# Performance work log

Hardware: AMD Instinct MI355X
Metric: run time of the kernel (lower is better)

Reference implementation:

```python
import jax, jax.numpy as jnp
import numpy as np

NUM_HEADS = 4
NUM_EXPERTS = 8
TOP_K = 2
AUX_W = 0.1


def setup_inputs() -> dict:
    key = jax.random.key(0)
    ks = jax.random.split(key, 16)
    B, W, C, T = 32, 64, 27, 2000
    E_EEG, H, S = 200, 256, 768
    D2 = 2 * H  # MoE input/hidden dim = 512
    s = 0.02

    def p(k, shape):
        return (jax.random.normal(k, shape, jnp.float32) * s)

    z = lambda *shape: jnp.zeros(shape, jnp.float32)
    return {
        "eeg_windows": jax.random.normal(ks[0], (B, W, C, T), jnp.float32),
        "padding_mask": jnp.zeros((B, W), bool),
        "smiles_emb": jax.random.normal(ks[1], (B, S), jnp.float32),
        # window encoder (linear stand-in): flatten (C*T) -> E_EEG
        "enc_W": p(ks[2], (C * T, E_EEG)), "enc_b": z(E_EEG),
        # aggregator (masked-mean + linear stand-in): E_EEG -> H
        "agg_W": p(ks[3], (E_EEG, H)), "agg_b": z(H),
        # smiles projection
        "smiles_W": p(ks[4], (S, H)), "smiles_b": z(H),
        # cross attention
        "Wq": p(ks[5], (H, H)), "bq": z(H),
        "Wk": p(ks[6], (H, H)), "bk": z(H),
        "Wv": p(ks[7], (H, H)), "bv": z(H),
        "Wo": p(ks[8], (H, H)), "bo": z(H),
        # MoE gate + experts
        "gate_W": p(ks[9], (D2, NUM_EXPERTS)), "gate_b": z(NUM_EXPERTS),
        "exp_W1": p(ks[10], (NUM_EXPERTS, D2, D2)), "exp_b1": z(NUM_EXPERTS, D2),
        "exp_W2": p(ks[11], (NUM_EXPERTS, D2, H)), "exp_b2": z(NUM_EXPERTS, H),
        # classifier
        "ln_g": jnp.ones((H,), jnp.float32), "ln_b": z(H),
        "cls_W": p(ks[12], (H, 2)), "cls_b": z(2),
    }


def reference(eeg_windows, padding_mask, smiles_emb, enc_W, enc_b, agg_W, agg_b,
              smiles_W, smiles_b, Wq, bq, Wk, bk, Wv, bv, Wo, bo,
              gate_W, gate_b, exp_W1, exp_b1, exp_W2, exp_b2,
              ln_g, ln_b, cls_W, cls_b):
    B, W, C, T = eeg_windows.shape
    H = agg_W.shape[1]
    dh = H // NUM_HEADS

    # --- window encoding (stand-in linear encoder) ---
    wemb = eeg_windows.reshape(B, W, C * T) @ enc_W + enc_b  # (B, W, E_EEG)

    # --- aggregator: masked mean pool over windows, then project ---
    valid = (~padding_mask).astype(wemb.dtype)[..., None]      # (B, W, 1)
    pooled = (wemb * valid).sum(1) / jnp.maximum(valid.sum(1), 1.0)
    eeg_emb = pooled @ agg_W + agg_b                           # (B, H)

    smiles_proj = smiles_emb @ smiles_W + smiles_b             # (B, H)

    # --- cross attention (single query token over single kv token) ---
    q = (eeg_emb @ Wq + bq).reshape(B, NUM_HEADS, dh)
    k = (smiles_proj @ Wk + bk).reshape(B, NUM_HEADS, dh)
    v = (smiles_proj @ Wv + bv).reshape(B, NUM_HEADS, dh)
    scores = (q * k).sum(-1, keepdims=True) / jnp.sqrt(jnp.float32(dh))
    attn = jnp.exp(scores - scores)  # softmax over a single key == 1
    attended = (attn * v).reshape(B, H) @ Wo + bo              # (B, H)

    fused = jnp.concatenate([attended, smiles_proj], axis=-1)  # (B, 2H)

    # --- sparse MoE: dense experts, top-k gate, gather, combine ---
    gate_probs = jax.nn.softmax(fused @ gate_W + gate_b, axis=-1)  # (B, E)
    topk_p, topk_i = jax.lax.top_k(gate_probs, TOP_K)
    topk_p = topk_p / topk_p.sum(-1, keepdims=True)
    h1 = jax.nn.gelu(jnp.einsum('bd,edh->beh', fused, exp_W1) + exp_b1,
                     approximate=False)
    expert_out = jnp.einsum('beh,eho->beo', h1, exp_W2) + exp_b2   # (B, E, H)
    sel = jnp.take_along_axis(expert_out, topk_i[:, :, None], axis=1)
    moe_out = (sel * topk_p[..., None]).sum(1)                     # (B, H)

    usage = gate_probs.mean(0)
    uniform = jnp.ones_like(usage) / usage.shape[-1]
    aux = (usage * jnp.log(uniform) - jnp.log(usage) * uniform).sum()

    # --- classifier: LayerNorm + Linear ---
    mu = moe_out.mean(-1, keepdims=True)
    var = moe_out.var(-1, keepdims=True)
    xn = (moe_out - mu) / jnp.sqrt(var + 1e-5)
    logits = (xn * ln_g + ln_b) @ cls_W + cls_b                    # (B, 2)
    return logits, aux * AUX_W
```

## Files before the change

### kernel.cpp

```cpp
#include <hip/hip_runtime.h>
#include <math.h>

#define HD 256
#define SD 768
#define D2 512
#define NE 8
#define NB 32
#define NBLK 256
#define NTHR 256
#define SFP 516

typedef float f32x4 __attribute__((ext_vector_type(4)));
typedef unsigned u32x4 __attribute__((ext_vector_type(4)));

__device__ __forceinline__ float gelu_exact(float x) {
    return 0.5f * x * (1.0f + erff(x * 0.70710678118654752f));
}

__device__ __forceinline__ void cstf(float* p, float v) {
    __hip_atomic_store(p, v, __ATOMIC_RELAXED, __HIP_MEMORY_SCOPE_AGENT);
}
__device__ __forceinline__ float cldf(const float* p) {
    return __hip_atomic_load(p, __ATOMIC_RELAXED, __HIP_MEMORY_SCOPE_AGENT);
}
__device__ __forceinline__ void csti(int* p, int v) {
    __hip_atomic_store(p, v, __ATOMIC_RELAXED, __HIP_MEMORY_SCOPE_AGENT);
}
__device__ __forceinline__ int cldi(const int* p) {
    return __hip_atomic_load(p, __ATOMIC_RELAXED, __HIP_MEMORY_SCOPE_AGENT);
}

__device__ __forceinline__ void stage16k(const float* __restrict__ gsrc,
                                         float* __restrict__ lds, int t)
{
    const f32x4* src = (const f32x4*)gsrc;
    f32x4 r[16];
    #pragma unroll
    for (int j = 0; j < 16; ++j) {
        const f32x4* p = src + (t + j * 256);
        asm volatile("global_load_dwordx4 %0, %1, off sc0 sc1"
                     : "=v"(r[j]) : "v"(p));
    }
    asm volatile("s_waitcnt vmcnt(0)" ::: "memory");
    __builtin_amdgcn_sched_barrier(0);
    #pragma unroll
    for (int j = 0; j < 16; ++j) {
        int q = t + j * 256;
        *(f32x4*)&lds[(q >> 7) * SFP + (q & 127) * 4] = r[j];
    }
}

__device__ __forceinline__ void gsync(unsigned* slots, unsigned* gen,
                                      unsigned tok) {
    __syncthreads();
    const int t = threadIdx.x;
    if (t == 0)
        __hip_atomic_store(slots + blockIdx.x, tok, __ATOMIC_RELAXED,
                           __HIP_MEMORY_SCOPE_AGENT);
    if (blockIdx.x == 0) {
        if (t < 64) {
            const u32x4* p = (const u32x4*)slots + t;
            for (;;) {
                u32x4 v;
                asm volatile("global_load_dwordx4 %0, %1, off sc0 sc1\n\t"
                             "s_waitcnt vmcnt(0)"
                             : "=&v"(v) : "v"(p) : "memory");
                bool ok = (v[0] == tok) & (v[1] == tok) &
                          (v[2] == tok) & (v[3] == tok);
                if (__ballot(ok) == ~0ull) break;
                __builtin_amdgcn_s_sleep(1);
            }
            if (t == 0)
                __hip_atomic_store(gen, tok, __ATOMIC_RELAXED,
                                   __HIP_MEMORY_SCOPE_AGENT);
        }
    } else {
        if (t == 0) {
            while (__hip_atomic_load(gen, __ATOMIC_RELAXED,
                                     __HIP_MEMORY_SCOPE_AGENT) != tok)
                __builtin_amdgcn_s_sleep(1);
        }
    }
    __builtin_amdgcn_fence(__ATOMIC_ACQUIRE, "workgroup");
    __syncthreads();
}

#define S_F     0
#define S_W     16512
#define S_R2    (16512 + 8192)
#define S_RED   (16512 + 8192 + 2048)
#define S_SMALL (16512 + 8192 + 2048 + 256)
#define SMEM_F  (16512 + 8192 + 2048 + 256 + 16)

__global__ __launch_bounds__(256) void fused_all(
    const float* __restrict__ smiles,
    const float* __restrict__ sW, const float* __restrict__ sb,
    const float* __restrict__ Wv, const float* __restrict__ bv,
    const float* __restrict__ Wo, const float* __restrict__ bo,
    const float* __restrict__ gW, const float* __restrict__ gb,
    const float* __restrict__ W1, const float* __restrict__ b1,
    const float* __restrict__ W2, const float* __restrict__ b2,
    const float* __restrict__ lng, const float* __restrict__ lnb,
    const float* __restrict__ clsW, const float* __restrict__ clsb,
    float* __restrict__ proj, float* __restrict__ fused,
    float* __restrict__ probs, float* __restrict__ pn,
    int* __restrict__ sel, float* __restrict__ h1,
    float* __restrict__ eo, unsigned* __restrict__ slots,
    unsigned* __restrict__ gen, unsigned* __restrict__ LC,
    float* __restrict__ out)
{
    __shared__ __align__(16) float smem[SMEM_F];
    __shared__ unsigned s_lc;
    const int bid = blockIdx.x, t = threadIdx.x;

    if (t == 0)
        s_lc = __hip_atomic_load(LC, __ATOMIC_RELAXED, __HIP_MEMORY_SCOPE_AGENT);
    __syncthreads();
    const unsigned tb = s_lc * 2654435761u;

    {
        int r = bid >> 3, sl = bid & 7;
        float* s_in = smem + S_F;
        float* s_red = smem + S_RED;
        const float* srow = smiles + (size_t)r * SD;
        for (int i = t; i < SD / 4; i += NTHR)
            ((float4*)s_in)[i] = ((const float4*)srow)[i];
        __syncthreads();
        int c = t & 31, kq = t >> 5;
        float acc = 0.f;
        const float* wp = sW + (size_t)(kq * 96) * HD + sl * 32 + c;
        #pragma unroll 8
        for (int k = 0; k < 96; ++k)
            acc = fmaf(s_in[kq * 96 + k], wp[(size_t)k * HD], acc);
        s_red[t] = acc;
        __syncthreads();
        if (t < 32) {
            float s = 0.f;
            #pragma unroll
            for (int q = 0; q < 8; ++q) s += s_red[q * 32 + t];
            int col = sl * 32 + t;
            s += sb[col];
            cstf(proj + r * HD + col, s);
            cstf(fused + (size_t)r * 2 * HD + HD + col, s);
        }
    }
    gsync(slots + 0 * NBLK, gen + 0, tb + 1u);

    if (bid < NB) {
        int b = bid;
        float* s_p   = smem + S_F;
        float* s_v   = smem + S_F + 256;
        float* s_f2  = smem + S_F + 512;
        float* s_acc = smem + S_R2;
        float* s_red = smem + S_RED;
        float* s_gate = smem + S_SMALL;
        s_p[t] = cldf(proj + b * HD + t);
        __syncthreads();
        int ks = t >> 6, cg = t & 63;

        f32x4 av = {0.f, 0.f, 0.f, 0.f};
        #pragma unroll 16
        for (int kk = 0; kk < 64; ++kk) {
            int k = ks * 64 + kk;
            f32x4 w = *(const f32x4*)(Wv + (size_t)k * HD + cg * 4);
            av += s_p[k] * w;
        }
        *(f32x4*)&s_acc[ks * 256 + cg * 4] = av;
        __syncthreads();
        s_v[t] = s_acc[t] + s_acc[256 + t] + s_acc[512 + t] + s_acc[768 + t]
               + bv[t];
        __syncthreads();

        f32x4 ao = {0.f, 0.f, 0.f, 0.f};
        #pragma unroll 16
        for (int kk = 0; kk < 64; ++kk) {
            int k = ks * 64 + kk;
            f32x4 w = *(const f32x4*)(Wo + (size_t)k * HD + cg * 4);
            ao += s_v[k] * w;
        }
        *(f32x4*)&s_acc[ks * 256 + cg * 4] = ao;
        __syncthreads();
        float att = s_acc[t] + s_acc[256 + t] + s_acc[512 + t] + s_acc[768 + t]
                  + bo[t];
        s_f2[t] = att;
        s_f2[HD + t] = s_p[t];
        cstf(fused + (size_t)b * 2 * HD + t, att);
        __syncthreads();

        int e = t & 7, ch = t >> 3;
        float gp = 0.f;
        #pragma unroll
        for (int j = 0; j < 16; ++j) {
            int d = ch * 16 + j;
            gp = fmaf(s_f2[d], gW[d * NE + e], gp);
        }
        s_red[t] = gp;
        __syncthreads();
        for (int off = 128; off >= 8; off >>= 1) {
            if (t < off) s_red[t] += s_red[t + off];
            __syncthreads();
        }
        if (t < NE) s_gate[t] = s_red[t] + gb[t];
        __syncthreads();
        if (t == 0) {
            float m = s_gate[0];
            for (int i = 1; i < NE; ++i) m = fmaxf(m, s_gate[i]);
            float ex[NE], ssum = 0.f;
            for (int i = 0; i < NE; ++i) { ex[i] = expf(s_gate[i] - m); ssum += ex[i]; }
            float pr[NE];
            for (int i = 0; i < NE; ++i) { pr[i] = ex[i] / ssum; cstf(probs + b * NE + i, pr[i]); }
            int i1 = 0;
            for (int i = 1; i < NE; ++i) if (pr[i] > pr[i1]) i1 = i;
            int i2 = (i1 == 0) ? 1 : 0;
            for (int i = 0; i < NE; ++i) if (i != i1 && pr[i] > pr[i2]) i2 = i;
            float p1 = pr[i1], p2 = pr[i2], s12 = p1 + p2;
            csti(sel + b * 2 + 0, i1);
            csti(sel + b * 2 + 1, i2);
            cstf(pn + b * 2 + 0, p1 / s12);
            cstf(pn + b * 2 + 1, p2 / s12);
        }
    }
    gsync(slots + 1 * NBLK, gen + 1, tb + 2u);

    {
        int e = bid >> 5, ct = bid & 31;
        float* s_f  = smem + S_F;
        float* s_w  = smem + S_W;
        float* s_r2 = smem + S_R2;
        stage16k(fused, s_f, t);
        {
            const float* Wb = W1 + (size_t)e * D2 * D2 + ct * 16;
            #pragma unroll
            for (int j = 0; j < 8; ++j) {
                int q = t + j * 256;
                int k = q >> 2, c4 = (q & 3) * 4;
                *(float4*)&s_w[k * 16 + c4] =
                    *(const float4*)(Wb + (size_t)k * D2 + c4);
            }
        }
        __syncthreads();
        int ks = t >> 6, l = t & 63;
        int rp = l >> 2, c4g = l & 3;
        int r0 = rp * 2, r1 = r0 + 1;
        const float* fr0 = s_f + r0 * SFP;
        const float* fr1 = s_f + r1 * SFP;
        const float* wb = s_w + c4g * 4;
        f32x4 a0 = {0.f, 0.f, 0.f, 0.f}, a1 = {0.f, 0.f, 0.f, 0.f};
        #pragma unroll 4
        for (int kq = 0; kq < 32; ++kq) {
            int k = ks * 128 + kq * 4;
            f32x4 w0 = *(const f32x4*)&wb[(k + 0) * 16];
            f32x4 w1 = *(const f32x4*)&wb[(k + 1) * 16];
            f32x4 w2 = *(const f32x4*)&wb[(k + 2) * 16];
            f32x4 w3 = *(const f32x4*)&wb[(k + 3) * 16];
            f32x4 f0 = *(const f32x4*)&fr0[k];
            f32x4 f1 = *(const f32x4*)&fr1[k];
            a0 += f0[0] * w0 + f0[1] * w1 + f0[2] * w2 + f0[3] * w3;
            a1 += f1[0] * w0 + f1[1] * w1 + f1[2] * w2 + f1[3] * w3;
        }
        int cl = c4g * 4;
        #pragma unroll
        for (int j = 0; j < 4; ++j) {
            s_r2[(r0 * 16 + cl + j) * 4 + ks] = a0[j];
            s_r2[(r1 * 16 + cl + j) * 4 + ks] = a1[j];
        }
        __syncthreads();
        #pragma unroll
        for (int o = 0; o < 2; ++o) {
            int outi = t * 2 + o;
            f32x4 p = *(const f32x4*)&s_r2[outi * 4];
            int r = outi >> 4, cl2 = outi & 15;
            int col = ct * 16 + cl2;
            float v = p[0] + p[1] + p[2] + p[3] + b1[e * D2 + col];
            cstf(h1 + ((size_t)e * NB + r) * D2 + col, gelu_exact(v));
        }
    }
    gsync(slots + 2 * NBLK, gen + 2, tb + 3u);

    if (bid < 128) {
        int e = bid >> 4, ct = bid & 15;
        float* s_h  = smem + S_F;
        float* s_w  = smem + S_W;
        float* s_r2 = smem + S_R2;
        stage16k(h1 + (size_t)e * NB * D2, s_h, t);
        {
            const float* Wb = W2 + (size_t)e * D2 * HD + ct * 16;
            #pragma unroll
            for (int j = 0; j < 8; ++j) {
                int q = t + j * 256;
                int k = q >> 2, c4 = (q & 3) * 4;
                *(float4*)&s_w[k * 16 + c4] =
                    *(const float4*)(Wb + (size_t)k * HD + c4);
            }
        }
        __syncthreads();
        int ks = t >> 6, l = t & 63;
        int rp = l >> 2, c4g = l & 3;
        int r0 = rp * 2, r1 = r0 + 1;
        const float* fr0 = s_h + r0 * SFP;
        const float* fr1 = s_h + r1 * SFP;
        const float* wb = s_w + c4g * 4;
        f32x4 a0 = {0.f, 0.f, 0.f, 0.f}, a1 = {0.f, 0.f, 0.f, 0.f};
        #pragma unroll 4
        for (int kq = 0; kq < 32; ++kq) {
            int k = ks * 128 + kq * 4;
            f32x4 w0 = *(const f32x4*)&wb[(k + 0) * 16];
            f32x4 w1 = *(const f32x4*)&wb[(k + 1) * 16];
            f32x4 w2 = *(const f32x4*)&wb[(k + 2) * 16];
            f32x4 w3 = *(const f32x4*)&wb[(k + 3) * 16];
            f32x4 f0 = *(const f32x4*)&fr0[k];
            f32x4 f1 = *(const f32x4*)&fr1[k];
            a0 += f0[0] * w0 + f0[1] * w1 + f0[2] * w2 + f0[3] * w3;
            a1 += f1[0] * w0 + f1[1] * w1 + f1[2] * w2 + f1[3] * w3;
        }
        int cl = c4g * 4;
        #pragma unroll
        for (int j = 0; j < 4; ++j) {
            s_r2[(r0 * 16 + cl + j) * 4 + ks] = a0[j];
            s_r2[(r1 * 16 + cl + j) * 4 + ks] = a1[j];
        }
        __syncthreads();
        #pragma unroll
        for (int o = 0; o < 2; ++o) {
            int outi = t * 2 + o;
            f32x4 p = *(const f32x4*)&s_r2[outi * 4];
            int r = outi >> 4, cl2 = outi & 15;
            int col = ct * 16 + cl2;
            float v = p[0] + p[1] + p[2] + p[3] + b2[e * HD + col];
            cstf(eo + ((size_t)e * NB + r) * HD + col, v);
        }
    }
    gsync(slots + 3 * NBLK, gen + 3, tb + 4u);

    if (bid == 0 && t == 0)
        __hip_atomic_store(LC, s_lc + 1u, __ATOMIC_RELAXED, __HIP_MEMORY_SCOPE_AGENT);

    if (bid < NB) {
        int b = bid;
        float* s_red = smem + S_RED;
        float* s_stats = smem + S_SMALL;
        int e0 = cldi(sel + b * 2 + 0), e1 = cldi(sel + b * 2 + 1);
        float p0 = cldf(pn + b * 2 + 0), p1 = cldf(pn + b * 2 + 1);
        float moe = p0 * cldf(eo + ((size_t)e0 * NB + b) * HD + t)
                  + p1 * cldf(eo + ((size_t)e1 * NB + b) * HD + t);

        s_red[t] = moe; __syncthreads();
        for (int off = 128; off > 0; off >>= 1) {
            if (t < off) s_red[t] += s_red[t + off];
            __syncthreads();
        }
        if (t == 0) s_stats[0] = s_red[0] * (1.f / HD);
        __syncthreads();
        float mu = s_stats[0];
        float d = moe - mu;

        s_red[t] = d * d; __syncthreads();
        for (int off = 128; off > 0; off >>= 1) {
            if (t < off) s_red[t] += s_red[t + off];
            __syncthreads();
        }
        if (t == 0) s_stats[1] = s_red[0] * (1.f / HD);
        __syncthreads();

        float xn = d * rsqrtf(s_stats[1] + 1e-5f);
        float y = fmaf(xn, lng[t], lnb[t]);

        s_red[t] = y * clsW[t * 2 + 0]; __syncthreads();
        for (int off = 128; off > 0; off >>= 1) {
            if (t < off) s_red[t] += s_red[t + off];
            __syncthreads();
        }
        if (t == 0) s_stats[2] = s_red[0] + clsb[0];
        __syncthreads();

        s_red[t] = y * clsW[t * 2 + 1]; __syncthreads();
        for (int off = 128; off > 0; off >>= 1) {
            if (t < off) s_red[t] += s_red[t + off];
            __syncthreads();
        }
        if (t == 0) {
            out[b * 2 + 0] = s_stats[2];
            out[b * 2 + 1] = s_red[0] + clsb[1];
        }

        if (bid == 0) {
            __syncthreads();
            s_red[t] = cldf(probs + t);
            __syncthreads();
            for (int off = 128; off >= 8; off >>= 1) {
                if (t < off) s_red[t] += s_red[t + off];
                __syncthreads();
            }
            if (t == 0) {
                float aux = 0.f;
                for (int e = 0; e < NE; ++e) {
                    float u = s_red[e] * (1.f / 32.f);
                    aux += u * logf(0.125f) - logf(u) * 0.125f;
                }
                out[64] = 0.1f * aux;
            }
        }
    }
}

extern "C" void kernel_launch(void* const* d_in, const int* in_sizes, int n_in,
                              void* d_out, int out_size, void* d_ws, size_t ws_size,
                              hipStream_t stream) {
    (void)in_sizes; (void)n_in; (void)out_size; (void)ws_size;
    const float* smiles = (const float*)d_in[2];
    const float* sW  = (const float*)d_in[7];
    const float* sb  = (const float*)d_in[8];
    const float* Wv  = (const float*)d_in[13];
    const float* bv  = (const float*)d_in[14];
    const float* Wo  = (const float*)d_in[15];
    const float* bo  = (const float*)d_in[16];
    const float* gW  = (const float*)d_in[17];
    const float* gb  = (const float*)d_in[18];
    const float* W1  = (const float*)d_in[19];
    const float* b1  = (const float*)d_in[20];
    const float* W2  = (const float*)d_in[21];
    const float* b2  = (const float*)d_in[22];
    const float* lng = (const float*)d_in[23];
    const float* lnb = (const float*)d_in[24];
    const float* cW  = (const float*)d_in[25];
    const float* cb  = (const float*)d_in[26];
    float* out = (float*)d_out;
    float* ws  = (float*)d_ws;

    float*    proj  = ws;
    float*    fused = ws + 8192;
    float*    probs = ws + 24576;
    float*    pn    = ws + 24832;
    int*      sel   = (int*)(ws + 24896);
    float*    h1    = ws + 24960;
    float*    eo    = ws + 156032;
    unsigned* slots = (unsigned*)(ws + 221568);
    unsigned* LC    = (unsigned*)(ws + 222592);
    unsigned* gen   = (unsigned*)(ws + 222593);

    fused_all<<<NBLK, NTHR, 0, stream>>>(
        smiles, sW, sb, Wv, bv, Wo, bo, gW, gb, W1, b1, W2, b2,
        lng, lnb, cW, cb,
        proj, fused, probs, pn, sel, h1, eo, slots, gen, LC, out);
}
```

Baseline: 41.64 us.

## Merge smiles projection into attention phase and compute only top-k expert W2

The smiles projection moves into the per-batch attention blocks, so 32 blocks each compute a full 768x256 projection row and one grid barrier is removed. The dense second expert layer and its barrier are also dropped. Each batch block now loads the h1 rows for its two selected experts, scales them by the gate weights and multiplies by those experts' W2 directly. This cuts the grid-wide syncs from four to two and skips the six unselected experts' W2 work. The cost is more serial per-block work, since 32 blocks stream sW and W2 from global memory instead of spreading that work across 256 blocks.

Result: slower. 48.03 us (+15.3%).

```diff
diff --git a/kernel.cpp b/kernel.cpp
--- a/kernel.cpp
+++ b/kernel.cpp
@@ -28,6 +28,12 @@
 }
 __device__ __forceinline__ int cldi(const int* p) {
     return __hip_atomic_load(p, __ATOMIC_RELAXED, __HIP_MEMORY_SCOPE_AGENT);
+}
+__device__ __forceinline__ f32x4 cld4(const float* p) {
+    f32x4 v;
+    asm volatile("global_load_dwordx4 %0, %1, off sc0 sc1\n\t"
+                 "s_waitcnt vmcnt(0)" : "=&v"(v) : "v"(p) : "memory");
+    return v;
 }
 
 __device__ __forceinline__ void stage16k(const float* __restrict__ gsrc,
@@ -102,10 +108,9 @@
     const float* __restrict__ W2, const float* __restrict__ b2,
     const float* __restrict__ lng, const float* __restrict__ lnb,
     const float* __restrict__ clsW, const float* __restrict__ clsb,
-    float* __restrict__ proj, float* __restrict__ fused,
-    float* __restrict__ probs, float* __restrict__ pn,
-    int* __restrict__ sel, float* __restrict__ h1,
-    float* __restrict__ eo, unsigned* __restrict__ slots,
+    float* __restrict__ fused, float* __restrict__ probs,
+    float* __restrict__ pn, int* __restrict__ sel,
+    float* __restrict__ h1, unsigned* __restrict__ slots,
     unsigned* __restrict__ gen, unsigned* __restrict__ LC,
     float* __restrict__ out)
 {
@@ -118,73 +123,74 @@
     __syncthreads();
     const unsigned tb = s_lc * 2654435761u;
 
-    {
-        int r = bid >> 3, sl = bid & 7;
-        float* s_in = smem + S_F;
-        float* s_red = smem + S_RED;
-        const float* srow = smiles + (size_t)r * SD;
-        for (int i = t; i < SD / 4; i += NTHR)
-            ((float4*)s_in)[i] = ((const float4*)srow)[i];
-        __syncthreads();
-        int c = t & 31, kq = t >> 5;
-        float acc = 0.f;
-        const float* wp = sW + (size_t)(kq * 96) * HD + sl * 32 + c;
-        #pragma unroll 8
-        for (int k = 0; k < 96; ++k)
-            acc = fmaf(s_in[kq * 96 + k], wp[(size_t)k * HD], acc);
-        s_red[t] = acc;
-        __syncthreads();
-        if (t < 32) {
-            float s = 0.f;
-            #pragma unroll
-            for (int q = 0; q < 8; ++q) s += s_red[q * 32 + t];
-            int col = sl * 32 + t;
-            s += sb[col];
-            cstf(proj + r * HD + col, s);
-            cstf(fused + (size_t)r * 2 * HD + HD + col, s);
-        }
-    }
-    gsync(slots + 0 * NBLK, gen + 0, tb + 1u);
-
     if (bid < NB) {
         int b = bid;
-        float* s_p   = smem + S_F;
-        float* s_v   = smem + S_F + 256;
-        float* s_f2  = smem + S_F + 512;
+        float* s_in  = smem + S_F;
+        float* s_p   = smem + S_F + 768;
+        float* s_v   = smem + S_F + 1024;
+        float* s_f2  = smem + S_F + 1280;
         float* s_acc = smem + S_R2;
         float* s_red = smem + S_RED;
         float* s_gate = smem + S_SMALL;
-        s_p[t] = cldf(proj + b * HD + t);
-        __syncthreads();
+
+        if (t < SD / 4)
+            *(f32x4*)&s_in[t * 4] = *(const f32x4*)(smiles + (size_t)b * SD + t * 4);
+        __syncthreads();
+
         int ks = t >> 6, cg = t & 63;
 
-        f32x4 av = {0.f, 0.f, 0.f, 0.f};
-        #pragma unroll 16
-        for (int kk = 0; kk < 64; ++kk) {
-            int k = ks * 64 + kk;
-            f32x4 w = *(const f32x4*)(Wv + (size_t)k * HD + cg * 4);
-            av += s_p[k] * w;
-        }
-        *(f32x4*)&s_acc[ks * 256 + cg * 4] = av;
+        {
+            f32x4 acc = {0.f, 0.f, 0.f, 0.f};
+            #pragma unroll 8
+            for (int kk = 0; kk < 192; ++kk) {
+                int k = ks * 192 + kk;
+                f32x4 w = *(const f32x4*)(sW + (size_t)k * HD + cg * 4);
+                acc += s_in[k] * w;
+            }
+            *(f32x4*)&s_acc[ks * 256 + cg * 4] = acc;
+        }
+        __syncthreads();
+        {
+            float p = s_acc[t] + s_acc[256 + t] + s_acc[512 + t] + s_acc[768 + t]
+                    + sb[t];
+            s_p[t] = p;
+            s_f2[HD + t] = p;
+            cstf(fused + (size_t)b * 2 * HD + HD + t, p);
+        }
+        __syncthreads();
+
+        {
+            f32x4 av = {0.f, 0.f, 0.f, 0.f};
+            #pragma unroll 16
+            for (int kk = 0; kk < 64; ++kk) {
+                int k = ks * 64 + kk;
+                f32x4 w = *(const f32x4*)(Wv + (size_t)k * HD + cg * 4);
+                av += s_p[k] * w;
+            }
+            *(f32x4*)&s_acc[ks * 256 + cg * 4] = av;
+        }
         __syncthreads();
         s_v[t] = s_acc[t] + s_acc[256 + t] + s_acc[512 + t] + s_acc[768 + t]
                + bv[t];
         __syncthreads();
 
-        f32x4 ao = {0.f, 0.f, 0.f, 0.f};
-        #pragma unroll 16
-        for (int kk = 0; kk < 64; ++kk) {
-            int k = ks * 64 + kk;
-            f32x4 w = *(const f32x4*)(Wo + (size_t)k * HD + cg * 4);
-            ao += s_v[k] * w;
-        }
-        *(f32x4*)&s_acc[ks * 256 + cg * 4] = ao;
-        __syncthreads();
-        float att = s_acc[t] + s_acc[256 + t] + s_acc[512 + t] + s_acc[768 + t]
-                  + bo[t];
-        s_f2[t] = att;
-        s_f2[HD + t] = s_p[t];
-        cstf(fused + (size_t)b * 2 * HD + t, att);
+        {
+            f32x4 ao = {0.f, 0.f, 0.f, 0.f};
+            #pragma unroll 16
+            for (int kk = 0; kk < 64; ++kk) {
+                int k = ks * 64 + kk;
+                f32x4 w = *(const f32x4*)(Wo + (size_t)k * HD + cg * 4);
+                ao += s_v[k] * w;
+            }
+            *(f32x4*)&s_acc[ks * 256 + cg * 4] = ao;
+        }
+        __syncthreads();
+        {
+            float att = s_acc[t] + s_acc[256 + t] + s_acc[512 + t] + s_acc[768 + t]
+                      + bo[t];
+            s_f2[t] = att;
+            cstf(fused + (size_t)b * 2 * HD + t, att);
+        }
         __syncthreads();
 
         int e = t & 7, ch = t >> 3;
@@ -220,7 +226,7 @@
             cstf(pn + b * 2 + 1, p2 / s12);
         }
     }
-    gsync(slots + 1 * NBLK, gen + 1, tb + 2u);
+    gsync(slots + 0 * NBLK, gen + 0, tb + 1u);
 
     {
         int e = bid >> 5, ct = bid & 31;
@@ -275,74 +281,64 @@
             cstf(h1 + ((size_t)e * NB + r) * D2 + col, gelu_exact(v));
         }
     }
-    gsync(slots + 2 * NBLK, gen + 2, tb + 3u);
-
-    if (bid < 128) {
-        int e = bid >> 4, ct = bid & 15;
-        float* s_h  = smem + S_F;
-        float* s_w  = smem + S_W;
-        float* s_r2 = smem + S_R2;
-        stage16k(h1 + (size_t)e * NB * D2, s_h, t);
-        {
-            const float* Wb = W2 + (size_t)e * D2 * HD + ct * 16;
-            #pragma unroll
-            for (int j = 0; j < 8; ++j) {
-                int q = t + j * 256;
-                int k = q >> 2, c4 = (q & 3) * 4;
-                *(float4*)&s_w[k * 16 + c4] =
-                    *(const float4*)(Wb + (size_t)k * HD + c4);
-            }
-        }
-        __syncthreads();
-        int ks = t >> 6, l = t & 63;
-        int rp = l >> 2, c4g = l & 3;
-        int r0 = rp * 2, r1 = r0 + 1;
-        const float* fr0 = s_h + r0 * SFP;
-        const float* fr1 = s_h + r1 * SFP;
-        const float* wb = s_w + c4g * 4;
-        f32x4 a0 = {0.f, 0.f, 0.f, 0.f}, a1 = {0.f, 0.f, 0.f, 0.f};
+    gsync(slots + 1 * NBLK, gen + 1, tb + 2u);
+
+    if (bid == 0 && t == 0)
+        __hip_atomic_store(LC, s_lc + 1u, __ATOMIC_RELAXED, __HIP_MEMORY_SCOPE_AGENT);
+
+    if (bid < NB) {
+        int b = bid;
+        float* s_h0 = smem + S_F;
+        float* s_h1 = smem + S_F + 512;
+        float* s_acc = smem + S_R2;
+        float* s_red = smem + S_RED;
+        float* s_stats = smem + S_SMALL;
+
+        int e0 = cldi(sel + b * 2 + 0), e1 = cldi(sel + b * 2 + 1);
+        float p0 = cldf(pn + b * 2 + 0), p1 = cldf(pn + b * 2 + 1);
+
+        {
+            int q = t & 127;
+            const float* src = (t < 128)
+                ? h1 + ((size_t)e0 * NB + b) * D2 + q * 4
+                : h1 + ((size_t)e1 * NB + b) * D2 + q * 4;
+            f32x4 v = cld4(src);
+            float pp = (t < 128) ? p0 : p1;
+            float* dst = (t < 128) ? &s_h0[q * 4] : &s_h1[q * 4];
+            v *= pp;
+            *(f32x4*)dst = v;
+        }
+        __syncthreads();
+
+        int ks = t >> 6, cg = t & 63;
+        const float* Wb0 = W2 + (size_t)e0 * D2 * HD + cg * 4;
+        const float* Wb1 = W2 + (size_t)e1 * D2 * HD + cg * 4;
+        f32x4 acc = {0.f, 0.f, 0.f, 0.f};
         #pragma unroll 4
         for (int kq = 0; kq < 32; ++kq) {
             int k = ks * 128 + kq * 4;
-            f32x4 w0 = *(const f32x4*)&wb[(k + 0) * 16];
-            f32x4 w1 = *(const f32x4*)&wb[(k + 1) * 16];
-            f32x4 w2 = *(const f32x4*)&wb[(k + 2) * 16];
-            f32x4 w3 = *(const f32x4*)&wb[(k + 3) * 16];
-            f32x4 f0 = *(const f32x4*)&fr0[k];
-            f32x4 f1 = *(const f32x4*)&fr1[k];
-            a0 += f0[0] * w0 + f0[1] * w1 + f0[2] * w2 + f0[3] * w3;
-            a1 += f1[0] * w0 + f1[1] * w1 + f1[2] * w2 + f1[3] * w3;
-        }
-        int cl = c4g * 4;
-        #pragma unroll
-        for (int j = 0; j < 4; ++j) {
-            s_r2[(r0 * 16 + cl + j) * 4 + ks] = a0[j];
-            s_r2[(r1 * 16 + cl + j) * 4 + ks] = a1[j];
-        }
-        __syncthreads();
-        #pragma unroll
-        for (int o = 0; o < 2; ++o) {
-            int outi = t * 2 + o;
-            f32x4 p = *(const f32x4*)&s_r2[outi * 4];
-            int r = outi >> 4, cl2 = outi & 15;
-            int col = ct * 16 + cl2;
-            float v = p[0] + p[1] + p[2] + p[3] + b2[e * HD + col];
-            cstf(eo + ((size_t)e * NB + r) * HD + col, v);
-        }
-    }
-    gsync(slots + 3 * NBLK, gen + 3, tb + 4u);
-
-    if (bid == 0 && t == 0)
-        __hip_atomic_store(LC, s_lc + 1u, __ATOMIC_RELAXED, __HIP_MEMORY_SCOPE_AGENT);
-
-    if (bid < NB) {
-        int b = bid;
-        float* s_red = smem + S_RED;
-        float* s_stats = smem + S_SMALL;
-        int e0 = cldi(sel + b * 2 + 0), e1 = cldi(sel + b * 2 + 1);
-        float p0 = cldf(pn + b * 2 + 0), p1 = cldf(pn + b * 2 + 1);
-        float moe = p0 * cldf(eo + ((size_t)e0 * NB + b) * HD + t)
-                  + p1 * cldf(eo + ((size_t)e1 * NB + b) * HD + t);
+            f32x4 h = *(const f32x4*)&s_h0[k];
+            f32x4 w0 = *(const f32x4*)(Wb0 + (size_t)(k + 0) * HD);
+            f32x4 w1 = *(const f32x4*)(Wb0 + (size_t)(k + 1) * HD);
+            f32x4 w2 = *(const f32x4*)(Wb0 + (size_t)(k + 2) * HD);
+            f32x4 w3 = *(const f32x4*)(Wb0 + (size_t)(k + 3) * HD);
+            acc += h[0] * w0 + h[1] * w1 + h[2] * w2 + h[3] * w3;
+        }
+        #pragma unroll 4
+        for (int kq = 0; kq < 32; ++kq) {
+            int k = ks * 128 + kq * 4;
+            f32x4 h = *(const f32x4*)&s_h1[k];
+            f32x4 w0 = *(const f32x4*)(Wb1 + (size_t)(k + 0) * HD);
+            f32x4 w1 = *(const f32x4*)(Wb1 + (size_t)(k + 1) * HD);
+            f32x4 w2 = *(const f32x4*)(Wb1 + (size_t)(k + 2) * HD);
+            f32x4 w3 = *(const f32x4*)(Wb1 + (size_t)(k + 3) * HD);
+            acc += h[0] * w0 + h[1] * w1 + h[2] * w2 + h[3] * w3;
+        }
+        *(f32x4*)&s_acc[ks * 256 + cg * 4] = acc;
+        __syncthreads();
+
+        float moe = s_acc[t] + s_acc[256 + t] + s_acc[512 + t] + s_acc[768 + t]
+                  + p0 * b2[e0 * HD + t] + p1 * b2[e1 * HD + t];
 
         s_red[t] = moe; __syncthreads();
         for (int off = 128; off > 0; off >>= 1) {
@@ -427,19 +423,17 @@
     float* out = (float*)d_out;
     float* ws  = (float*)d_ws;
 
-    float*    proj  = ws;
-    float*    fused = ws + 8192;
-    float*    probs = ws + 24576;
-    float*    pn    = ws + 24832;
-    int*      sel   = (int*)(ws + 24896);
-    float*    h1    = ws + 24960;
-    float*    eo    = ws + 156032;
-    unsigned* slots = (unsigned*)(ws + 221568);
-    unsigned* LC    = (unsigned*)(ws + 222592);
-    unsigned* gen   = (unsigned*)(ws + 222593);
+    float*    fused = ws;
+    float*    probs = ws + 16384;
+    float*    pn    = ws + 16640;
+    int*      sel   = (int*)(ws + 16704);
+    float*    h1    = ws + 16768;
+    unsigned* slots = (unsigned*)(ws + 147840);
+    unsigned* LC    = (unsigned*)(ws + 148352);
+    unsigned* gen   = (unsigned*)(ws + 148353);
 
     fused_all<<<NBLK, NTHR, 0, stream>>>(
         smiles, sW, sb, Wv, bv, Wo, bo, gW, gb, W1, b1, W2, b2,
         lng, lnb, cW, cb,
-        proj, fused, probs, pn, sel, h1, eo, slots, gen, LC, out);
-}
+        fused, probs, pn, sel, h1, slots, gen, LC, out);
+}
```

## Replace global barriers with targeted producer-consumer slot waits

Applied to the files above, without the earlier changes.

Swaps the full grid barrier (block 0 gathers all slots, then broadcasts a generation flag) for per-stage flag posting, where each consumer block polls only the slots of the producer blocks it depends on. Blocks that have no work left in later stages now exit early. The aim is to cut barrier latency and the serial gather-then-broadcast step through block 0. The cost is more polling traffic from many blocks, and correctness now depends on each block's dependency sets being right, including the LC counter update at the end.

Result: slower. 44.01 us (+5.7%).

```diff
diff --git a/kernel.cpp b/kernel.cpp
--- a/kernel.cpp
+++ b/kernel.cpp
@@ -50,35 +50,25 @@
     }
 }
 
-__device__ __forceinline__ void gsync(unsigned* slots, unsigned* gen,
-                                      unsigned tok) {
+__device__ __forceinline__ void post_slot(unsigned* slots, unsigned tok) {
     __syncthreads();
-    const int t = threadIdx.x;
-    if (t == 0)
+    if (threadIdx.x == 0)
         __hip_atomic_store(slots + blockIdx.x, tok, __ATOMIC_RELAXED,
                            __HIP_MEMORY_SCOPE_AGENT);
-    if (blockIdx.x == 0) {
-        if (t < 64) {
-            const u32x4* p = (const u32x4*)slots + t;
-            for (;;) {
-                u32x4 v;
-                asm volatile("global_load_dwordx4 %0, %1, off sc0 sc1\n\t"
-                             "s_waitcnt vmcnt(0)"
-                             : "=&v"(v) : "v"(p) : "memory");
-                bool ok = (v[0] == tok) & (v[1] == tok) &
-                          (v[2] == tok) & (v[3] == tok);
-                if (__ballot(ok) == ~0ull) break;
-                __builtin_amdgcn_s_sleep(1);
-            }
-            if (t == 0)
-                __hip_atomic_store(gen, tok, __ATOMIC_RELAXED,
-                                   __HIP_MEMORY_SCOPE_AGENT);
-        }
-    } else {
-        if (t == 0) {
-            while (__hip_atomic_load(gen, __ATOMIC_RELAXED,
-                                     __HIP_MEMORY_SCOPE_AGENT) != tok)
-                __builtin_amdgcn_s_sleep(1);
+}
+
+__device__ __forceinline__ void wait_slots(const unsigned* slots, int nq,
+                                           unsigned tok) {
+    if (threadIdx.x < 64 && (int)threadIdx.x < nq) {
+        const u32x4* p = (const u32x4*)slots + threadIdx.x;
+        for (;;) {
+            u32x4 v;
+            asm volatile("global_load_dwordx4 %0, %1, off sc0 sc1\n\t"
+                         "s_waitcnt vmcnt(0)"
+                         : "=&v"(v) : "v"(p) : "memory");
+            if ((v[0] == tok) & (v[1] == tok) & (v[2] == tok) & (v[3] == tok))
+                break;
+            __builtin_amdgcn_s_sleep(2);
         }
     }
     __builtin_amdgcn_fence(__ATOMIC_ACQUIRE, "workgroup");
@@ -105,9 +95,10 @@
     float* __restrict__ proj, float* __restrict__ fused,
     float* __restrict__ probs, float* __restrict__ pn,
     int* __restrict__ sel, float* __restrict__ h1,
-    float* __restrict__ eo, unsigned* __restrict__ slots,
-    unsigned* __restrict__ gen, unsigned* __restrict__ LC,
-    float* __restrict__ out)
+    float* __restrict__ eo,
+    unsigned* __restrict__ slot0, unsigned* __restrict__ slot1,
+    unsigned* __restrict__ slot2, unsigned* __restrict__ slot3,
+    unsigned* __restrict__ LC, float* __restrict__ out)
 {
     __shared__ __align__(16) float smem[SMEM_F];
     __shared__ unsigned s_lc;
@@ -144,9 +135,10 @@
             cstf(fused + (size_t)r * 2 * HD + HD + col, s);
         }
     }
-    gsync(slots + 0 * NBLK, gen + 0, tb + 1u);
+    post_slot(slot0, tb + 1u);
 
     if (bid < NB) {
+        wait_slots(slot0 + bid * 8, 2, tb + 1u);
         int b = bid;
         float* s_p   = smem + S_F;
         float* s_v   = smem + S_F + 256;
@@ -219,9 +211,10 @@
             cstf(pn + b * 2 + 0, p1 / s12);
             cstf(pn + b * 2 + 1, p2 / s12);
         }
-    }
-    gsync(slots + 1 * NBLK, gen + 1, tb + 2u);
-
+        post_slot(slot1, tb + 2u);
+    }
+
+    wait_slots(slot1, 8, tb + 2u);
     {
         int e = bid >> 5, ct = bid & 31;
         float* s_f  = smem + S_F;
@@ -275,10 +268,12 @@
             cstf(h1 + ((size_t)e * NB + r) * D2 + col, gelu_exact(v));
         }
     }
-    gsync(slots + 2 * NBLK, gen + 2, tb + 3u);
-
-    if (bid < 128) {
+    post_slot(slot2, tb + 3u);
+    if (bid >= 128) return;
+
+    {
         int e = bid >> 4, ct = bid & 15;
+        wait_slots(slot2 + e * 32, 8, tb + 3u);
         float* s_h  = smem + S_F;
         float* s_w  = smem + S_W;
         float* s_r2 = smem + S_R2;
@@ -330,12 +325,11 @@
             cstf(eo + ((size_t)e * NB + r) * HD + col, v);
         }
     }
-    gsync(slots + 3 * NBLK, gen + 3, tb + 4u);
-
-    if (bid == 0 && t == 0)
-        __hip_atomic_store(LC, s_lc + 1u, __ATOMIC_RELAXED, __HIP_MEMORY_SCOPE_AGENT);
-
-    if (bid < NB) {
+    post_slot(slot3, tb + 4u);
+    if (bid >= NB) return;
+
+    wait_slots(slot3, 32, tb + 4u);
+    {
         int b = bid;
         float* s_red = smem + S_RED;
         float* s_stats = smem + S_SMALL;
@@ -400,6 +394,13 @@
                 out[64] = 0.1f * aux;
             }
         }
+    }
+
+    if (bid == 0) {
+        wait_slots(slot0, 64, tb + 1u);
+        if (t == 0)
+            __hip_atomic_store(LC, s_lc + 1u, __ATOMIC_RELAXED,
+                               __HIP_MEMORY_SCOPE_AGENT);
     }
 }
 
@@ -434,12 +435,15 @@
     int*      sel   = (int*)(ws + 24896);
     float*    h1    = ws + 24960;
     float*    eo    = ws + 156032;
-    unsigned* slots = (unsigned*)(ws + 221568);
-    unsigned* LC    = (unsigned*)(ws + 222592);
-    unsigned* gen   = (unsigned*)(ws + 222593);
+    unsigned* slot0 = (unsigned*)(ws + 221568);
+    unsigned* slot1 = (unsigned*)(ws + 221824);
+    unsigned* slot2 = (unsigned*)(ws + 221888);
+    unsigned* slot3 = (unsigned*)(ws + 222144);
+    unsigned* LC    = (unsigned*)(ws + 222272);
 
     fused_all<<<NBLK, NTHR, 0, stream>>>(
         smiles, sW, sb, Wv, bv, Wo, bo, gW, gb, W1, b1, W2, b2,
         lng, lnb, cW, cb,
-        proj, fused, probs, pn, sel, h1, eo, slots, gen, LC, out);
-}
+        proj, fused, probs, pn, sel, h1, eo,
+        slot0, slot1, slot2, slot3, LC, out);
+}
```
